# Optimization experiments

Hardware: AMD Instinct MI355X
Metric: run time of the kernel (lower is better)

Reference implementation:

```python
import jax, jax.numpy as jnp
import numpy as np

B, N, M, K = 4, 8192, 2048, 8
F1, F2 = 256, 256


def _knn_idx(p1t, p2t, k):
    # p1t [B,N,3], p2t [B,M,3] -> idx [B,N,k] of k nearest points in p2t for each p1t point
    d = (jnp.sum(p1t ** 2, -1)[:, :, None]
         + jnp.sum(p2t ** 2, -1)[:, None, :]
         - 2.0 * jnp.einsum('bnc,bmc->bnm', p1t, p2t))
    _, idx = jax.lax.top_k(-d, k)
    return idx


def _gather(feat, idx):
    # feat [B,C,M], idx [B,N,K] -> [B,C,N,K]  (grouping_operation)
    return jax.vmap(lambda f, i: f[:, i])(feat, idx)


def setup_inputs() -> dict:
    key = jax.random.key(0)
    ks = jax.random.split(key, 16)
    rn = lambda k, s: jax.random.normal(k, s, dtype=jnp.float32)
    ru = lambda k, s: jax.random.uniform(k, s, dtype=jnp.float32)
    return {
        'pos1': rn(ks[0], (B, 3, N)),
        'pos2': rn(ks[1], (B, 3, M)),
        'feature1': rn(ks[2], (B, F1, N)),
        'feature2': rn(ks[3], (B, F2, M)),
        'w1_0': rn(ks[4], (128, F2 + 3)) * 0.05, 's1_0': ru(ks[5], (128,)), 'b1_0': rn(ks[6], (128,)) * 0.05,
        'w1_1': rn(ks[7], (128, 128)) * 0.05, 's1_1': ru(ks[8], (128,)), 'b1_1': rn(ks[9], (128,)) * 0.05,
        'w1_2': rn(ks[10], (256, 128)) * 0.05, 's1_2': ru(ks[11], (256,)), 'b1_2': rn(ks[12], (256,)) * 0.05,
        'w2_0': rn(ks[13], (256, 256 + F1)) * 0.05, 's2_0': ru(ks[14], (256,)), 'b2_0': rn(ks[15], (256,)) * 0.05,
    }


def reference(pos1, pos2, feature1, feature2,
              w1_0, s1_0, b1_0, w1_1, s1_1, b1_1, w1_2, s1_2, b1_2,
              w2_0, s2_0, b2_0):
    # KNN grouping (knn=True branch): neighbors of each pos1 point among pos2 points
    idx = _knn_idx(pos1.transpose(0, 2, 1), pos2.transpose(0, 2, 1), K)  # [B,N,K]
    pos2_grouped = _gather(pos2, idx)                 # [B,3,N,K]
    pos_diff = pos2_grouped - pos1[:, :, :, None]     # [B,3,N,K]
    feat2_grouped = _gather(feature2, idx)            # [B,F2,N,K]
    feat = jnp.concatenate([feat2_grouped, pos_diff], axis=1)  # [B,F2+3,N,K]
    # mlp1: 1x1 Conv2d (no bias) + BN(eval, folded scale/bias) + ReLU
    for w, s, b in ((w1_0, s1_0, b1_0), (w1_1, s1_1, b1_1), (w1_2, s1_2, b1_2)):
        feat = jax.nn.relu(jnp.einsum('oc,bcnk->bonk', w, feat)
                           * s[None, :, None, None] + b[None, :, None, None])
    feat = jnp.max(feat, axis=-1)                     # [B,256,N]
    feat = jnp.concatenate([feat, feature1], axis=1)  # [B,256+F1,N]
    # mlp2: 1x1 Conv1d (no bias) + BN + ReLU
    for w, s, b in ((w2_0, s2_0, b2_0),):
        feat = jax.nn.relu(jnp.einsum('oc,bcn->bon', w, feat)
                           * s[None, :, None] + b[None, :, None])
    return feat
```

## Files before the change

### kernel.cpp

```cpp
#include <hip/hip_runtime.h>
#include <hip/hip_bf16.h>

#define B_ 4
#define N_ 8192
#define M_ 2048
#define K_ 8

typedef __bf16 bf16x8 __attribute__((ext_vector_type(8)));
typedef __bf16 bf16x4 __attribute__((ext_vector_type(4)));
typedef float  floatx4 __attribute__((ext_vector_type(4)));
typedef unsigned long long u64k;

#define AS1G __attribute__((address_space(1)))
#define AS3L __attribute__((address_space(3)))

__device__ __forceinline__ void ce(u64k& a, u64k& b) {
  u64k lo = a < b ? a : b;
  u64k hi = a < b ? b : a;
  a = lo; b = hi;
}

__device__ __forceinline__ void merge8(u64k (&a)[8], const u64k (&c)[8]) {
  #pragma unroll
  for (int k = 0; k < 8; k++) { u64k x = c[7 - k]; a[k] = a[k] < x ? a[k] : x; }
  ce(a[0], a[4]); ce(a[1], a[5]); ce(a[2], a[6]); ce(a[3], a[7]);
  ce(a[0], a[2]); ce(a[1], a[3]); ce(a[4], a[6]); ce(a[5], a[7]);
  ce(a[0], a[1]); ce(a[2], a[3]); ce(a[4], a[5]); ce(a[6], a[7]);
}

__global__ __launch_bounds__(256) void pre_knn(
    const float* __restrict__ w10, const float* __restrict__ w11,
    const float* __restrict__ w12, const float* __restrict__ w20,
    const float* __restrict__ feature1, const float* __restrict__ feature2,
    const float* __restrict__ pos1, const float* __restrict__ pos2,
    __bf16* __restrict__ w0p, __bf16* __restrict__ w11b,
    __bf16* __restrict__ w12b, __bf16* __restrict__ w20b,
    __bf16* __restrict__ f2t, __bf16* __restrict__ f1t,
    u64k* __restrict__ part)
{
  __shared__ __align__(16) char smem[24576];
  const int bid = blockIdx.x;
  const int tid = threadIdx.x;

  if (bid < 2048) {
    floatx4* P = (floatx4*)smem;
    u64k (*md)[32] = (u64k(*)[32])(smem + 8192);
    const int b = (bid >> 7) & 3;
    const int quarter = bid >> 9;
    const int n0 = (bid & 127) * 64;
    const int cbase = quarter * 512;

    const float* p2 = pos2 + b * 3 * M_;
    for (int i = tid; i < 512; i += 256) {
      const int c = cbase + i;
      float x = p2[c], y = p2[M_ + c], z = p2[2 * M_ + c];
      floatx4 q;
      q[0] = x; q[1] = y; q[2] = z;
      q[3] = __fadd_rn(__fadd_rn(__fmul_rn(x, x), __fmul_rn(y, y)), __fmul_rn(z, z));
      P[i] = q;
    }
    __syncthreads();

    const int p = tid >> 2, t = tid & 3;
    const int n = n0 + p;
    const float* p1 = pos1 + b * 3 * N_;
    const float x1 = p1[n], y1 = p1[N_ + n], z1 = p1[2 * N_ + n];
    const float r1 = __fadd_rn(__fadd_rn(__fmul_rn(x1, x1), __fmul_rn(y1, y1)),
                               __fmul_rn(z1, z1));

    u64k bd[8];
    #pragma unroll
    for (int r = 0; r < 8; r++) bd[r] = ~0ULL;

    for (int bb = 0; bb < 16; ++bb) {
      floatx4 q[8];
      #pragma unroll
      for (int i = 0; i < 8; i++) q[i] = P[4 * (8 * bb + i) + t];

      u64k s[8];
      #pragma unroll
      for (int i = 0; i < 8; i++) {
        float dot = __fadd_rn(__fadd_rn(__fmul_rn(x1, q[i][0]), __fmul_rn(y1, q[i][1])),
                              __fmul_rn(z1, q[i][2]));
        float d = __fsub_rn(__fadd_rn(r1, q[i][3]), __fmul_rn(2.0f, dot));
        unsigned du = __float_as_uint(d);
        unsigned k32 = du ^ ((unsigned)((int)du >> 31) | 0x80000000u);
        s[i] = ((u64k)k32 << 11) | (unsigned)(cbase + 4 * (8 * bb + i) + t);
      }

      ce(s[0], s[1]); ce(s[2], s[3]); ce(s[4], s[5]); ce(s[6], s[7]);
      ce(s[0], s[2]); ce(s[1], s[3]); ce(s[4], s[6]); ce(s[5], s[7]);
      ce(s[1], s[2]); ce(s[5], s[6]);
      ce(s[0], s[4]); ce(s[1], s[5]); ce(s[2], s[6]); ce(s[3], s[7]);
      ce(s[2], s[4]); ce(s[3], s[5]);
      ce(s[1], s[2]); ce(s[3], s[4]); ce(s[5], s[6]);

      if (s[0] < bd[7]) merge8(bd, s);
    }

    {
      const int swp = (p & 3) << 3;
      #pragma unroll
      for (int r = 0; r < 8; r++) md[p][(t * 8 + r) ^ swp] = bd[r];
    }
    __syncthreads();

    if (tid < 64) {
      const int sw = tid & 3;
      const int b0 = (0 ^ sw) << 3, b1 = (1 ^ sw) << 3;
      const int b2 = (2 ^ sw) << 3, b3 = (3 ^ sw) << 3;
      int h0 = 0, h1 = 0, h2 = 0, h3 = 0;
      u64k* o = part + ((size_t)((b * 4 + quarter) * N_ + n0 + tid)) * 8;
      #pragma unroll
      for (int r = 0; r < 8; r++) {
        u64k k0 = md[tid][b0 + h0], k1 = md[tid][b1 + h1];
        u64k k2 = md[tid][b2 + h2], k3 = md[tid][b3 + h3];
        u64k m01 = k0 < k1 ? k0 : k1;
        u64k m23 = k2 < k3 ? k2 : k3;
        u64k m = m01 < m23 ? m01 : m23;
        h0 += (k0 == m); h1 += (k1 == m); h2 += (k2 == m); h3 += (k3 == m);
        o[r] = m;
      }
    }
  } else if (bid < 4096) {
    float (*tile)[33] = (float(*)[33])smem;
    const int tb = bid - 2048;
    const int C = 256, L = M_;
    const int b = tb >> 9;
    const int c0 = ((tb >> 6) & 7) * 32, l0 = (tb & 63) * 32;
    const int tx = tid & 31, ty = tid >> 5;
    const float* src = feature2 + (size_t)b * C * L;
    #pragma unroll
    for (int i = 0; i < 4; i++)
      tile[ty + 8 * i][tx] = src[(size_t)(c0 + ty + 8 * i) * L + l0 + tx];
    __syncthreads();
    __bf16* dst = f2t + (size_t)b * L * C;
    #pragma unroll
    for (int i = 0; i < 4; i++)
      dst[(size_t)(l0 + ty + 8 * i) * C + c0 + tx] = (__bf16)tile[tx][ty + 8 * i];
  } else if (bid < 12288) {
    float (*tile)[33] = (float(*)[33])smem;
    const int tb = bid - 4096;
    const int C = 256, L = N_;
    const int b = tb >> 11;
    const int c0 = ((tb >> 8) & 7) * 32, l0 = (tb & 255) * 32;
    const int tx = tid & 31, ty = tid >> 5;
    const float* src = feature1 + (size_t)b * C * L;
    #pragma unroll
    for (int i = 0; i < 4; i++)
      tile[ty + 8 * i][tx] = src[(size_t)(c0 + ty + 8 * i) * L + l0 + tx];
    __syncthreads();
    __bf16* dst = f1t + (size_t)b * L * C;
    #pragma unroll
    for (int i = 0; i < 4; i++)
      dst[(size_t)(l0 + ty + 8 * i) * C + c0 + tx] = (__bf16)tile[tx][ty + 8 * i];
  } else {
    int t = (bid - 12288) * 256 + tid;
    if (t < 36864) {
      int o = t / 288, c = t - o * 288;
      w0p[t] = (c < 259) ? (__bf16)w10[o * 259 + c] : (__bf16)0.0f;
    } else if (t < 53248) {
      int i = t - 36864; w11b[i] = (__bf16)w11[i];
    } else if (t < 86016) {
      int i = t - 53248; w12b[i] = (__bf16)w12[i];
    } else if (t < 217088) {
      int i = t - 86016; w20b[i] = (__bf16)w20[i];
    }
  }
}

__global__ __launch_bounds__(256) void knn_merge(
    const u64k* __restrict__ part, int* __restrict__ idx_out)
{
  const int pt = blockIdx.x * 256 + threadIdx.x;
  const int b = pt >> 13, n = pt & (N_ - 1);
  u64k a01[8], c1[8], a23[8], c3[8];
  {
    const u64k* l0 = part + ((size_t)((b * 4 + 0) * N_ + n)) * 8;
    const u64k* l1 = part + ((size_t)((b * 4 + 1) * N_ + n)) * 8;
    const u64k* l2 = part + ((size_t)((b * 4 + 2) * N_ + n)) * 8;
    const u64k* l3 = part + ((size_t)((b * 4 + 3) * N_ + n)) * 8;
    #pragma unroll
    for (int r = 0; r < 8; r++) {
      a01[r] = l0[r]; c1[r] = l1[r]; a23[r] = l2[r]; c3[r] = l3[r];
    }
  }
  merge8(a01, c1);
  merge8(a23, c3);
  merge8(a01, a23);
  int* o = idx_out + (size_t)pt * 8;
  #pragma unroll
  for (int r = 0; r < 8; r++) o[r] = (int)(a01[r] & 2047u);
}

template <int KSTEPS>
__device__ __forceinline__ void mfma_kloop_swz(
    const __bf16* X, const __bf16* W, int wstride, int c0, int lane,
    floatx4 (&acc)[4][2])
{
  const int lrow = lane & 15, quad = lane >> 4;
  const floatx4 fz = {0.f, 0.f, 0.f, 0.f};
  #pragma unroll
  for (int pt = 0; pt < 4; pt++) { acc[pt][0] = fz; acc[pt][1] = fz; }

  bf16x8 wf0 = *(const bf16x8*)(W + (size_t)(c0 + lrow) * wstride + quad * 8);
  bf16x8 wf1 = *(const bf16x8*)(W + (size_t)(c0 + 16 + lrow) * wstride + quad * 8);
  bf16x8 xf[4];
  #pragma unroll
  for (int pt = 0; pt < 4; pt++) {
    const int row = pt * 16 + lrow;
    xf[pt] = *(const bf16x8*)((const char*)X + row * 256
                              + ((quad * 16) ^ ((row & 7) << 4)));
  }

  #pragma unroll
  for (int ks = 0; ks < KSTEPS; ks++) {
    bf16x8 wn0, wn1, xn[4];
    if (ks + 1 < KSTEPS) {
      const int kn = (ks + 1) * 32 + quad * 8;
      wn0 = *(const bf16x8*)(W + (size_t)(c0 + lrow) * wstride + kn);
      wn1 = *(const bf16x8*)(W + (size_t)(c0 + 16 + lrow) * wstride + kn);
      #pragma unroll
      for (int pt = 0; pt < 4; pt++) {
        const int row = pt * 16 + lrow;
        xn[pt] = *(const bf16x8*)((const char*)X + row * 256
                                  + (((ks + 1) * 64 + quad * 16) ^ ((row & 7) << 4)));
      }
    }
    #pragma unroll
    for (int pt = 0; pt < 4; pt++) {
      acc[pt][0] = __builtin_amdgcn_mfma_f32_16x16x32_bf16(wf0, xf[pt], acc[pt][0], 0, 0, 0);
      acc[pt][1] = __builtin_amdgcn_mfma_f32_16x16x32_bf16(wf1, xf[pt], acc[pt][1], 0, 0, 0);
    }
    if (ks + 1 < KSTEPS) {
      wf0 = wn0; wf1 = wn1;
      #pragma unroll
      for (int pt = 0; pt < 4; pt++) xf[pt] = xn[pt];
    }
  }
}

__global__ __launch_bounds__(256, 3) void mlp1_kernel(
    const float* __restrict__ pos1, const float* __restrict__ pos2,
    const int* __restrict__ idx, const __bf16* __restrict__ f2t,
    const __bf16* __restrict__ w0p, const float* __restrict__ s10, const float* __restrict__ b10,
    const __bf16* __restrict__ w11b, const float* __restrict__ s11, const float* __restrict__ b11,
    const __bf16* __restrict__ w12b, const float* __restrict__ s12, const float* __restrict__ b12,
    __bf16* __restrict__ maxed)
{
  __shared__ __align__(16) __bf16 Xs[64 * 256];
  __bf16* const Y1 = Xs;
  __bf16* const Y0 = Xs + 32 * 256;
  __bf16* const Mst = Xs + 32 * 256;

  const int b = blockIdx.y;
  const int n0 = blockIdx.x * 8;
  const int tid = threadIdx.x;
  const int wave = tid >> 6, lane = tid & 63;
  const int lrow = lane & 15, quad = lane >> 4;
  const int c0 = 32 * wave;
  const int idxbase = (b * N_ + n0) * K_;

  {
    const int r0 = wave * 16;
    const int hf = lane >> 5;
    const int ch = lane & 31;
    int mr[8];
    #pragma unroll
    for (int i = 0; i < 8; i++)
      mr[i] = idx[idxbase + r0 + 2 * i + hf];
    #pragma unroll
    for (int i = 0; i < 8; i++) {
      const int r = r0 + 2 * i + hf;
      const char* src = (const char*)f2t
          + (((size_t)(b * M_ + mr[i])) << 9)
          + ((ch << 4) ^ ((r & 7) << 4));
      __builtin_amdgcn_global_load_lds(
          (const AS1G unsigned int*)src,
          (AS3L unsigned int*)(Xs + (r0 + 2 * i) * 256),
          16, 0, 0);
    }
  }

  bf16x8 xlast[4];
  #pragma unroll
  for (int pt = 0; pt < 4; pt++) { bf16x8 v = {}; xlast[pt] = v; }
  if (quad == 0) {
    #pragma unroll
    for (int pt = 0; pt < 4; pt++) {
      const int r = pt * 16 + lrow;
      const int m = idx[idxbase + r];
      const int n = n0 + (r >> 3);
      bf16x8 v = {};
      v[0] = (__bf16)(pos2[b * 3 * M_ + m]          - pos1[b * 3 * N_ + n]);
      v[1] = (__bf16)(pos2[b * 3 * M_ + M_ + m]     - pos1[b * 3 * N_ + N_ + n]);
      v[2] = (__bf16)(pos2[b * 3 * M_ + 2 * M_ + m] - pos1[b * 3 * N_ + 2 * N_ + n]);
      xlast[pt] = v;
    }
  }

  bf16x8 wf0 = *(const bf16x8*)(w0p + (size_t)(c0 + lrow) * 288 + quad * 8);
  bf16x8 wf1 = *(const bf16x8*)(w0p + (size_t)(c0 + 16 + lrow) * 288 + quad * 8);

  __syncthreads();

  floatx4 acc[4][2];
  {
    const floatx4 fz = {0.f, 0.f, 0.f, 0.f};
    #pragma unroll
    for (int pt = 0; pt < 4; pt++) { acc[pt][0] = fz; acc[pt][1] = fz; }

    const int swz = (lrow & 7) << 4;
    bf16x8 xf[4];
    #pragma unroll
    for (int pt = 0; pt < 4; pt++)
      xf[pt] = *(const bf16x8*)((const char*)Xs + (pt * 16 + lrow) * 512
                                + ((quad * 16) ^ swz));

    #pragma unroll
    for (int ks = 0; ks < 9; ks++) {
      bf16x8 wn0, wn1, xn[4];
      if (ks < 8) {
        const int kn = (ks + 1) * 32 + quad * 8;
        wn0 = *(const bf16x8*)(w0p + (size_t)(c0 + lrow) * 288 + kn);
        wn1 = *(const bf16x8*)(w0p + (size_t)(c0 + 16 + lrow) * 288 + kn);
        if (ks < 7) {
          const int kb = ((ks + 1) * 64 + quad * 16) ^ swz;
          #pragma unroll
          for (int pt = 0; pt < 4; pt++)
            xn[pt] = *(const bf16x8*)((const char*)Xs + (pt * 16 + lrow) * 512 + kb);
        } else {
          #pragma unroll
          for (int pt = 0; pt < 4; pt++) xn[pt] = xlast[pt];
        }
      }
      #pragma unroll
      for (int pt = 0; pt < 4; pt++) {
        acc[pt][0] = __builtin_amdgcn_mfma_f32_16x16x32_bf16(wf0, xf[pt], acc[pt][0], 0, 0, 0);
        acc[pt][1] = __builtin_amdgcn_mfma_f32_16x16x32_bf16(wf1, xf[pt], acc[pt][1], 0, 0, 0);
      }
      if (ks < 8) {
        wf0 = wn0; wf1 = wn1;
        #pragma unroll
        for (int pt = 0; pt < 4; pt++) xf[pt] = xn[pt];
      }
    }
  }

  __syncthreads();

  #pragma unroll
  for (int pt = 0; pt < 4; pt++) {
    #pragma unroll
    for (int wt = 0; wt < 2; wt++) {
      const int colg = c0 + wt * 16 + quad * 4;
      floatx4 s4 = *(const floatx4*)(s10 + colg);
      floatx4 b4 = *(const floatx4*)(b10 + colg);
      bf16x4 pk;
      #pragma unroll
      for (int r = 0; r < 4; r++) {
        float v = acc[pt][wt][r] * s4[r] + b4[r];
        pk[r] = (__bf16)(v > 0.f ? v : 0.f);
      }
      const int row = pt * 16 + lrow;
      const int cb = colg * 2;
      *(bf16x4*)((char*)Y0 + row * 256
                 + ((cb & ~15) ^ ((row & 7) << 4)) + (cb & 15)) = pk;
    }
  }
  __syncthreads();

  {
    floatx4 a1c[4][2];
    mfma_kloop_swz<4>(Y0, w11b, 128, c0, lane, a1c);
    #pragma unroll
    for (int pt = 0; pt < 4; pt++) {
      #pragma unroll
      for (int wt = 0; wt < 2; wt++) {
        const int colg = c0 + wt * 16 + quad * 4;
        floatx4 s4 = *(const floatx4*)(s11 + colg);
        floatx4 b4 = *(const floatx4*)(b11 + colg);
        bf16x4 pk;
        #pragma unroll
        for (int r = 0; r < 4; r++) {
          float v = a1c[pt][wt][r] * s4[r] + b4[r];
          pk[r] = (__bf16)(v > 0.f ? v : 0.f);
        }
        const int row = pt * 16 + lrow;
        const int cb = colg * 2;
        *(bf16x4*)((char*)Y1 + row * 256
                   + ((cb & ~15) ^ ((row & 7) << 4)) + (cb & 15)) = pk;
      }
    }
  }
  __syncthreads();

  #pragma unroll
  for (int p = 0; p < 2; p++) {
    floatx4 a2c[4][2];
    mfma_kloop_swz<4>(Y1, w12b, 128, 128 * p + c0, lane, a2c);
    #pragma unroll
    for (int pt = 0; pt < 4; pt++) {
      #pragma unroll
      for (int wt = 0; wt < 2; wt++) {
        const int colg = 128 * p + c0 + wt * 16 + quad * 4;
        floatx4 s4 = *(const floatx4*)(s12 + colg);
        floatx4 b4 = *(const floatx4*)(b12 + colg);
        floatx4 v;
        #pragma unroll
        for (int r = 0; r < 4; r++) {
          float t = a2c[pt][wt][r] * s4[r] + b4[r];
          v[r] = t > 0.f ? t : 0.f;
        }
        #pragma unroll
        for (int st = 1; st <= 4; st <<= 1) {
          #pragma unroll
          for (int r = 0; r < 4; r++)
            v[r] = fmaxf(v[r], __shfl_xor(v[r], st, 64));
        }
        if ((lrow & 7) == 0) {
          const int point = pt * 2 + (lrow >> 3);
          bf16x4 pk;
          #pragma unroll
          for (int r = 0; r < 4; r++) pk[r] = (__bf16)v[r];
          *(bf16x4*)(Mst + point * 264 + colg) = pk;
        }
      }
    }
  }
  __syncthreads();

  {
    const int point = tid >> 5, ch = tid & 31;
    bf16x8 v = *(const bf16x8*)(Mst + point * 264 + ch * 8);
    *(bf16x8*)(maxed + ((size_t)(b * N_ + n0 + point)) * 256 + ch * 8) = v;
  }
}

__global__ __launch_bounds__(256, 3) void mlp2_kernel(
    const __bf16* __restrict__ maxed, const __bf16* __restrict__ f1t,
    const __bf16* __restrict__ w20b, const float* __restrict__ s20,
    const float* __restrict__ b20, float* __restrict__ out)
{
  __shared__ __align__(16) __bf16 As[2][32 * 256];
  const int rows0 = blockIdx.x * 32;
  const int b = rows0 >> 13;
  const int nbase = rows0 & (N_ - 1);
  const int tid = threadIdx.x;
  const int wave = tid >> 6, lane = tid & 63;
  const int lrow = lane & 15, quad = lane >> 4;
  const int c0 = 64 * wave;

  {
    const int r0 = wave * 8;
    const int hf = lane >> 5, ch = lane & 31;
    #pragma unroll
    for (int i = 0; i < 4; i++) {
      const int r = r0 + 2 * i + hf;
      const size_t srow = ((size_t)(rows0 + r)) << 9;
      const int so = (ch << 4) ^ ((r & 7) << 4);
      __builtin_amdgcn_global_load_lds(
          (const AS1G unsigned int*)((const char*)maxed + srow + so),
          (AS3L unsigned int*)(&As[0][(r0 + 2 * i) * 256]), 16, 0, 0);
      __builtin_amdgcn_global_load_lds(
          (const AS1G unsigned int*)((const char*)f1t + srow + so),
          (AS3L unsigned int*)(&As[1][(r0 + 2 * i) * 256]), 16, 0, 0);
    }
  }

  bf16x8 wf[4];
  #pragma unroll
  for (int wt = 0; wt < 4; wt++)
    wf[wt] = *(const bf16x8*)(w20b + (size_t)(c0 + wt * 16 + lrow) * 512 + quad * 8);

  __syncthreads();

  floatx4 acc[2][4];
  const floatx4 fz = {0.f, 0.f, 0.f, 0.f};
  #pragma unroll
  for (int mt = 0; mt < 2; mt++)
    #pragma unroll
    for (int wt = 0; wt < 4; wt++) acc[mt][wt] = fz;

  auto aaddr = [&](int ks, int mt) -> const char* {
    const int row = mt * 16 + lrow;
    return (const char*)(&As[ks >> 3][0]) + row * 512
           + ((((ks & 7) * 64) + quad * 16) ^ ((row & 7) << 4));
  };

  bf16x8 af[2];
  af[0] = *(const bf16x8*)aaddr(0, 0);
  af[1] = *(const bf16x8*)aaddr(0, 1);

  #pragma unroll
  for (int ks = 0; ks < 16; ks++) {
    bf16x8 wn[4], an[2];
    if (ks < 15) {
      const int kn = (ks + 1) * 32 + quad * 8;
      #pragma unroll
      for (int wt = 0; wt < 4; wt++)
        wn[wt] = *(const bf16x8*)(w20b + (size_t)(c0 + wt * 16 + lrow) * 512 + kn);
      an[0] = *(const bf16x8*)aaddr(ks + 1, 0);
      an[1] = *(const bf16x8*)aaddr(ks + 1, 1);
    }
    #pragma unroll
    for (int mt = 0; mt < 2; mt++)
      #pragma unroll
      for (int wt = 0; wt < 4; wt++)
        acc[mt][wt] = __builtin_amdgcn_mfma_f32_16x16x32_bf16(af[mt], wf[wt], acc[mt][wt], 0, 0, 0);
    if (ks < 15) {
      #pragma unroll
      for (int wt = 0; wt < 4; wt++) wf[wt] = wn[wt];
      af[0] = an[0]; af[1] = an[1];
    }
  }

  #pragma unroll
  for (int wt = 0; wt < 4; wt++) {
    const int col = c0 + wt * 16 + lrow;
    const float s = s20[col];
    const float bb = b20[col];
    #pragma unroll
    for (int mt = 0; mt < 2; mt++) {
      floatx4 pk;
      #pragma unroll
      for (int r = 0; r < 4; r++) {
        float v = acc[mt][wt][r] * s + bb;
        pk[r] = v > 0.f ? v : 0.f;
      }
      const int n = nbase + mt * 16 + quad * 4;
      *(floatx4*)(out + ((size_t)(b * 256 + col)) * N_ + n) = pk;
    }
  }
}

extern "C" void kernel_launch(void* const* d_in, const int* in_sizes, int n_in,
                              void* d_out, int out_size, void* d_ws, size_t ws_size,
                              hipStream_t stream)
{
  const float* pos1     = (const float*)d_in[0];
  const float* pos2     = (const float*)d_in[1];
  const float* feature1 = (const float*)d_in[2];
  const float* feature2 = (const float*)d_in[3];
  const float* w1_0 = (const float*)d_in[4];
  const float* s1_0 = (const float*)d_in[5];
  const float* b1_0 = (const float*)d_in[6];
  const float* w1_1 = (const float*)d_in[7];
  const float* s1_1 = (const float*)d_in[8];
  const float* b1_1 = (const float*)d_in[9];
  const float* w1_2 = (const float*)d_in[10];
  const float* s1_2 = (const float*)d_in[11];
  const float* b1_2 = (const float*)d_in[12];
  const float* w2_0 = (const float*)d_in[13];
  const float* s2_0 = (const float*)d_in[14];
  const float* b2_0 = (const float*)d_in[15];

  char* ws = (char*)d_ws;
  int*    idx   = (int*)(ws);
  __bf16* f2t   = (__bf16*)(ws + 1048576);
  __bf16* f1t   = (__bf16*)(ws + 5242880);
  __bf16* maxed = (__bf16*)(ws + 22020096);
  __bf16* w0p   = (__bf16*)(ws + 38797312);
  __bf16* w11b  = (__bf16*)(ws + 38871040);
  __bf16* w12b  = (__bf16*)(ws + 38903808);
  __bf16* w20b  = (__bf16*)(ws + 38969344);
  u64k*   part  = (u64k*)(ws + 22020096);

  pre_knn<<<dim3(13136), 256, 0, stream>>>(
      w1_0, w1_1, w1_2, w2_0, feature1, feature2, pos1, pos2,
      w0p, w11b, w12b, w20b, f2t, f1t, part);
  knn_merge<<<dim3(N_ * B_ / 256), 256, 0, stream>>>(part, idx);
  mlp1_kernel<<<dim3(N_ / 8, B_), 256, 0, stream>>>(
      pos1, pos2, idx, f2t, w0p, s1_0, b1_0, w11b, s1_1, b1_1, w12b, s1_2, b1_2, maxed);
  mlp2_kernel<<<dim3(N_ * B_ / 32), 256, 0, stream>>>(maxed, f1t, w20b, s2_0, b2_0,
                                                      (float*)d_out);
}
```

Measured before the change: 308.9 us.

## Restructure mlp1 LDS layout with padded buffers and LDS-based max reduction

Replaces the XOR-swizzled intermediate activation buffers in mlp1 with a separate padded (stride 136) LDS buffer, and folds the BN+ReLU epilogue into a shared layer helper. The K-neighbor max is now done by re-reading the last layer's output from LDS in 128 threads instead of cross-lane shuffles, with extra block barriers per half. KNN indices and position differences are precomputed once into LDS by the first 64 threads, which adds a barrier before the gather. LDS use per block grows, which may reduce occupancy under the 3-blocks-per-SM launch bound, and more synchronisation is added.

```diff
diff --git a/kernel.cpp b/kernel.cpp
--- a/kernel.cpp
+++ b/kernel.cpp
@@ -194,11 +194,13 @@
 }
 
 template <int KSTEPS>
-__device__ __forceinline__ void mfma_kloop_swz(
-    const __bf16* X, const __bf16* W, int wstride, int c0, int lane,
-    floatx4 (&acc)[4][2])
+__device__ __forceinline__ void mfma_layer_lds(
+    const __bf16* X, const __bf16* W, int wstride,
+    const float* sv, const float* bv,
+    __bf16* Y, int ycolbase, int c0, int lane)
 {
   const int lrow = lane & 15, quad = lane >> 4;
+  floatx4 acc[4][2];
   const floatx4 fz = {0.f, 0.f, 0.f, 0.f};
   #pragma unroll
   for (int pt = 0; pt < 4; pt++) { acc[pt][0] = fz; acc[pt][1] = fz; }
@@ -207,11 +209,8 @@
   bf16x8 wf1 = *(const bf16x8*)(W + (size_t)(c0 + 16 + lrow) * wstride + quad * 8);
   bf16x8 xf[4];
   #pragma unroll
-  for (int pt = 0; pt < 4; pt++) {
-    const int row = pt * 16 + lrow;
-    xf[pt] = *(const bf16x8*)((const char*)X + row * 256
-                              + ((quad * 16) ^ ((row & 7) << 4)));
-  }
+  for (int pt = 0; pt < 4; pt++)
+    xf[pt] = *(const bf16x8*)(X + (pt * 16 + lrow) * 136 + quad * 8);
 
   #pragma unroll
   for (int ks = 0; ks < KSTEPS; ks++) {
@@ -221,11 +220,8 @@
       wn0 = *(const bf16x8*)(W + (size_t)(c0 + lrow) * wstride + kn);
       wn1 = *(const bf16x8*)(W + (size_t)(c0 + 16 + lrow) * wstride + kn);
       #pragma unroll
-      for (int pt = 0; pt < 4; pt++) {
-        const int row = pt * 16 + lrow;
-        xn[pt] = *(const bf16x8*)((const char*)X + row * 256
-                                  + (((ks + 1) * 64 + quad * 16) ^ ((row & 7) << 4)));
-      }
+      for (int pt = 0; pt < 4; pt++)
+        xn[pt] = *(const bf16x8*)(X + (pt * 16 + lrow) * 136 + kn);
     }
     #pragma unroll
     for (int pt = 0; pt < 4; pt++) {
@@ -236,6 +232,23 @@
       wf0 = wn0; wf1 = wn1;
       #pragma unroll
       for (int pt = 0; pt < 4; pt++) xf[pt] = xn[pt];
+    }
+  }
+
+  #pragma unroll
+  for (int pt = 0; pt < 4; pt++) {
+    #pragma unroll
+    for (int wt = 0; wt < 2; wt++) {
+      const int colg = c0 + wt * 16 + quad * 4;
+      floatx4 s4 = *(const floatx4*)(sv + colg);
+      floatx4 b4 = *(const floatx4*)(bv + colg);
+      bf16x4 pk;
+      #pragma unroll
+      for (int r = 0; r < 4; r++) {
+        float v = acc[pt][wt][r] * s4[r] + b4[r];
+        pk[r] = (__bf16)(v > 0.f ? v : 0.f);
+      }
+      *(bf16x4*)(Y + (pt * 16 + lrow) * 136 + (colg - ycolbase)) = pk;
     }
   }
 }
@@ -249,9 +262,10 @@
     __bf16* __restrict__ maxed)
 {
   __shared__ __align__(16) __bf16 Xs[64 * 256];
+  __shared__ __align__(16) __bf16 Y0[64 * 136];
+  __shared__ int mrow[64];
+  __shared__ __align__(16) float dp[64][4];
   __bf16* const Y1 = Xs;
-  __bf16* const Y0 = Xs + 32 * 256;
-  __bf16* const Mst = Xs + 32 * 256;
 
   const int b = blockIdx.y;
   const int n0 = blockIdx.x * 8;
@@ -259,21 +273,29 @@
   const int wave = tid >> 6, lane = tid & 63;
   const int lrow = lane & 15, quad = lane >> 4;
   const int c0 = 32 * wave;
-  const int idxbase = (b * N_ + n0) * K_;
+
+  if (tid < 64) {
+    const int r = tid, g = r >> 3;
+    const int m = idx[(b * N_ + n0) * K_ + r];
+    mrow[r] = m;
+    const int n = n0 + g;
+    dp[r][0] = pos2[b * 3 * M_ + m]          - pos1[b * 3 * N_ + n];
+    dp[r][1] = pos2[b * 3 * M_ + M_ + m]     - pos1[b * 3 * N_ + N_ + n];
+    dp[r][2] = pos2[b * 3 * M_ + 2 * M_ + m] - pos1[b * 3 * N_ + 2 * N_ + n];
+    dp[r][3] = 0.f;
+  }
+  __syncthreads();
 
   {
     const int r0 = wave * 16;
-    const int hf = lane >> 5;
+    const int half = lane >> 5;
     const int ch = lane & 31;
-    int mr[8];
-    #pragma unroll
-    for (int i = 0; i < 8; i++)
-      mr[i] = idx[idxbase + r0 + 2 * i + hf];
     #pragma unroll
     for (int i = 0; i < 8; i++) {
-      const int r = r0 + 2 * i + hf;
+      const int r = r0 + 2 * i + half;
+      const int m = mrow[r];
       const char* src = (const char*)f2t
-          + (((size_t)(b * M_ + mr[i])) << 9)
+          + (((size_t)(b * M_ + m)) << 9)
           + ((ch << 4) ^ ((r & 7) << 4));
       __builtin_amdgcn_global_load_lds(
           (const AS1G unsigned int*)src,
@@ -284,19 +306,13 @@
 
   bf16x8 xlast[4];
   #pragma unroll
-  for (int pt = 0; pt < 4; pt++) { bf16x8 v = {}; xlast[pt] = v; }
-  if (quad == 0) {
-    #pragma unroll
-    for (int pt = 0; pt < 4; pt++) {
-      const int r = pt * 16 + lrow;
-      const int m = idx[idxbase + r];
-      const int n = n0 + (r >> 3);
-      bf16x8 v = {};
-      v[0] = (__bf16)(pos2[b * 3 * M_ + m]          - pos1[b * 3 * N_ + n]);
-      v[1] = (__bf16)(pos2[b * 3 * M_ + M_ + m]     - pos1[b * 3 * N_ + N_ + n]);
-      v[2] = (__bf16)(pos2[b * 3 * M_ + 2 * M_ + m] - pos1[b * 3 * N_ + 2 * N_ + n]);
-      xlast[pt] = v;
-    }
+  for (int pt = 0; pt < 4; pt++) {
+    bf16x8 v = {};
+    if (quad == 0) {
+      floatx4 d = *(const floatx4*)(&dp[pt * 16 + lrow][0]);
+      v[0] = (__bf16)d[0]; v[1] = (__bf16)d[1]; v[2] = (__bf16)d[2];
+    }
+    xlast[pt] = v;
   }
 
   bf16x8 wf0 = *(const bf16x8*)(w0p + (size_t)(c0 + lrow) * 288 + quad * 8);
@@ -304,8 +320,8 @@
 
   __syncthreads();
 
-  floatx4 acc[4][2];
   {
+    floatx4 acc[4][2];
     const floatx4 fz = {0.f, 0.f, 0.f, 0.f};
     #pragma unroll
     for (int pt = 0; pt < 4; pt++) { acc[pt][0] = fz; acc[pt][1] = fz; }
@@ -345,95 +361,53 @@
         for (int pt = 0; pt < 4; pt++) xf[pt] = xn[pt];
       }
     }
-  }
-
-  __syncthreads();
-
-  #pragma unroll
-  for (int pt = 0; pt < 4; pt++) {
-    #pragma unroll
-    for (int wt = 0; wt < 2; wt++) {
-      const int colg = c0 + wt * 16 + quad * 4;
-      floatx4 s4 = *(const floatx4*)(s10 + colg);
-      floatx4 b4 = *(const floatx4*)(b10 + colg);
-      bf16x4 pk;
-      #pragma unroll
-      for (int r = 0; r < 4; r++) {
-        float v = acc[pt][wt][r] * s4[r] + b4[r];
-        pk[r] = (__bf16)(v > 0.f ? v : 0.f);
-      }
-      const int row = pt * 16 + lrow;
-      const int cb = colg * 2;
-      *(bf16x4*)((char*)Y0 + row * 256
-                 + ((cb & ~15) ^ ((row & 7) << 4)) + (cb & 15)) = pk;
-    }
-  }
-  __syncthreads();
-
-  {
-    floatx4 a1c[4][2];
-    mfma_kloop_swz<4>(Y0, w11b, 128, c0, lane, a1c);
     #pragma unroll
     for (int pt = 0; pt < 4; pt++) {
       #pragma unroll
       for (int wt = 0; wt < 2; wt++) {
         const int colg = c0 + wt * 16 + quad * 4;
-        floatx4 s4 = *(const floatx4*)(s11 + colg);
-        floatx4 b4 = *(const floatx4*)(b11 + colg);
+        floatx4 s4 = *(const floatx4*)(s10 + colg);
+        floatx4 b4 = *(const floatx4*)(b10 + colg);
         bf16x4 pk;
         #pragma unroll
         for (int r = 0; r < 4; r++) {
-          float v = a1c[pt][wt][r] * s4[r] + b4[r];
+          float v = acc[pt][wt][r] * s4[r] + b4[r];
           pk[r] = (__bf16)(v > 0.f ? v : 0.f);
         }
-        const int row = pt * 16 + lrow;
-        const int cb = colg * 2;
-        *(bf16x4*)((char*)Y1 + row * 256
-                   + ((cb & ~15) ^ ((row & 7) << 4)) + (cb & 15)) = pk;
+        *(bf16x4*)(Y0 + (pt * 16 + lrow) * 136 + colg) = pk;
       }
     }
   }
   __syncthreads();
 
+  mfma_layer_lds<4>(Y0, w11b, 128, s11, b11, Y1, 0, c0, lane);
+  __syncthreads();
+
   #pragma unroll
   for (int p = 0; p < 2; p++) {
-    floatx4 a2c[4][2];
-    mfma_kloop_swz<4>(Y1, w12b, 128, 128 * p + c0, lane, a2c);
-    #pragma unroll
-    for (int pt = 0; pt < 4; pt++) {
-      #pragma unroll
-      for (int wt = 0; wt < 2; wt++) {
-        const int colg = 128 * p + c0 + wt * 16 + quad * 4;
-        floatx4 s4 = *(const floatx4*)(s12 + colg);
-        floatx4 b4 = *(const floatx4*)(b12 + colg);
-        floatx4 v;
+    mfma_layer_lds<4>(Y1, w12b, 128, s12, b12, Y0, 128 * p, 128 * p + c0, lane);
+    __syncthreads();
+    if (tid < 128) {
+      const int g = tid >> 4, cb = (tid & 15) * 8;
+      bf16x8 v0 = *(const bf16x8*)(Y0 + (g * 8) * 136 + cb);
+      float fmx[8];
+      #pragma unroll
+      for (int j = 0; j < 8; j++) fmx[j] = (float)v0[j];
+      #pragma unroll
+      for (int k = 1; k < 8; k++) {
+        bf16x8 v = *(const bf16x8*)(Y0 + (g * 8 + k) * 136 + cb);
         #pragma unroll
-        for (int r = 0; r < 4; r++) {
-          float t = a2c[pt][wt][r] * s4[r] + b4[r];
-          v[r] = t > 0.f ? t : 0.f;
+        for (int j = 0; j < 8; j++) {
+          float f = (float)v[j];
+          fmx[j] = f > fmx[j] ? f : fmx[j];
         }
-        #pragma unroll
-        for (int st = 1; st <= 4; st <<= 1) {
-          #pragma unroll
-          for (int r = 0; r < 4; r++)
-            v[r] = fmaxf(v[r], __shfl_xor(v[r], st, 64));
-        }
-        if ((lrow & 7) == 0) {
-          const int point = pt * 2 + (lrow >> 3);
-          bf16x4 pk;
-          #pragma unroll
-          for (int r = 0; r < 4; r++) pk[r] = (__bf16)v[r];
-          *(bf16x4*)(Mst + point * 264 + colg) = pk;
-        }
-      }
-    }
-  }
-  __syncthreads();
-
-  {
-    const int point = tid >> 5, ch = tid & 31;
-    bf16x8 v = *(const bf16x8*)(Mst + point * 264 + ch * 8);
-    *(bf16x8*)(maxed + ((size_t)(b * N_ + n0 + point)) * 256 + ch * 8) = v;
+      }
+      bf16x8 o;
+      #pragma unroll
+      for (int j = 0; j < 8; j++) o[j] = (__bf16)fmx[j];
+      *(bf16x8*)(maxed + ((size_t)(b * N_ + n0 + g)) * 256 + 128 * p + cb) = o;
+    }
+    __syncthreads();
   }
 }
 
```

After: 299.5 us. 3.0% less time.
